# Performance work log

Hardware: AMD Instinct MI355X
Metric: run time of the kernel (lower is better)

The kernel has to match this reference:

```python
import jax, jax.numpy as jnp
import numpy as np

N = 50000
E = 400000
C_IN = 32
H = 64
RATIO = 0.5
SEQ_LEN = 5


def setup_inputs() -> dict:
    key = jax.random.key(0)
    ks = jax.random.split(key, 12)
    x = jax.random.normal(ks[0], (N, C_IN), jnp.float32)
    row = jax.random.randint(ks[1], (E,), 0, N, jnp.int32)
    off = jax.random.randint(ks[2], (E,), 1, N, jnp.int32)
    col = ((row + off) % N).astype(jnp.int32)  # no self-loops
    edge_index = jnp.stack([row, col])
    mask = jax.random.uniform(ks[3], (N,)) < 0.5

    def g(k, shape, fan):
        return jax.random.normal(k, shape, jnp.float32) / np.float32(np.sqrt(fan))

    return {
        "x": x, "edge_index": edge_index, "mask": mask,
        "conv0_w": g(ks[4], (C_IN, H), C_IN), "conv0_b": jnp.zeros((H,), jnp.float32),
        "conv1_w": g(ks[5], (H, H), H), "conv1_b": jnp.zeros((H,), jnp.float32),
        "pool_w": g(ks[6], (H,), H),
        "up_w": g(ks[7], (H, H), H), "up_b": jnp.zeros((H,), jnp.float32),
        "lstm0_w_ih": g(ks[8], (4 * H, H), H), "lstm0_w_hh": g(ks[9], (4 * H, H), H),
        "lstm0_b_ih": jnp.zeros((4 * H,), jnp.float32), "lstm0_b_hh": jnp.zeros((4 * H,), jnp.float32),
        "fin_w_ih": g(ks[10], (4 * H, H), H), "fin_w_hh": g(ks[11], (4 * H, H), H),
        "fin_b_ih": jnp.zeros((4 * H,), jnp.float32), "fin_b_hh": jnp.zeros((4 * H,), jnp.float32),
    }


def _coalesce(row, col, w, n):
    # sum duplicate (row, col) entries; output sorted by (row, col)
    key = row.astype(np.int64) * n + col.astype(np.int64)
    uk, inv = np.unique(key, return_inverse=True)
    w2 = np.bincount(inv, weights=w.astype(np.float64), minlength=uk.shape[0]).astype(np.float32)
    return uk // n, uk % n, w2


def _augment_adj(row, col, w, n):
    # remove self loops, add self loops (weight 1), compute A @ A (sparse), remove self loops
    m = row != col
    row = np.concatenate([row[m].astype(np.int64), np.arange(n, dtype=np.int64)])
    col = np.concatenate([col[m].astype(np.int64), np.arange(n, dtype=np.int64)])
    w = np.concatenate([w[m].astype(np.float32), np.ones(n, np.float32)])
    row, col, w = _coalesce(row, col, w, n)  # CSR-ordered
    cnt = np.bincount(row, minlength=n)
    indptr = np.concatenate([[0], np.cumsum(cnt)])
    dk = cnt[col]                      # out-degree of middle node k for each edge (i,k)
    starts = indptr[col]
    total = int(dk.sum())
    seg = np.repeat(np.cumsum(dk) - dk, dk)
    gi = np.repeat(starts, dk) + (np.arange(total) - seg)
    oi = np.repeat(row, dk)
    oj = col[gi]
    ow = np.repeat(w, dk) * w[gi]
    r2, c2, w2 = _coalesce(oi, oj, ow, n)
    m2 = r2 != c2
    return r2[m2], c2[m2], w2[m2]


def _gcn(x, row, col, ew, n, W, b):
    # GCNConv(improved=True): self-loop weight 2.0, symmetric deg^-1/2 normalization,
    # aggregate messages at target (col)
    h = x @ W
    loop = jnp.arange(n, dtype=row.dtype)
    r = jnp.concatenate([row, loop])
    c = jnp.concatenate([col, loop])
    w = jnp.concatenate([ew, jnp.full((n,), 2.0, ew.dtype)])
    deg = jax.ops.segment_sum(w, c, num_segments=n)
    dinv = jnp.where(deg > 0, jax.lax.rsqrt(deg), 0.0)
    norm = dinv[r] * w * dinv[c]
    out = jax.ops.segment_sum(norm[:, None] * h[r], c, num_segments=n)
    return out + b


def _sequences(x, mi):
    # sliding window [idx-L+1, idx] per masked node, zero left-padded
    t = mi[:, None] + jnp.arange(SEQ_LEN)[None, :] - (SEQ_LEN - 1)  # [M, L]
    return jnp.where((t >= 0)[:, :, None], x[jnp.clip(t, 0)], 0.0)


def _lstm_last(seq, w_ih, w_hh, b_ih, b_hh):
    # torch LSTM gate order: i, f, g, o; zero init state; return last hidden
    h = jnp.zeros((seq.shape[0], w_hh.shape[1]), seq.dtype)
    c = jnp.zeros_like(h)
    def step(carry, xt):
        h, c = carry
        g = xt @ w_ih.T + h @ w_hh.T + b_ih + b_hh
        i, f, gg, o = jnp.split(g, 4, axis=-1)
        c = jax.nn.sigmoid(f) * c + jax.nn.sigmoid(i) * jnp.tanh(gg)
        h = jax.nn.sigmoid(o) * jnp.tanh(c)
        return (h, c), None
    (h, _), _ = jax.lax.scan(step, (h, c), jnp.swapaxes(seq, 0, 1))
    return h


def reference(x, edge_index, mask, conv0_w, conv0_b, conv1_w, conv1_b, pool_w,
              up_w, up_b, lstm0_w_ih, lstm0_w_hh, lstm0_b_ih, lstm0_b_hh,
              fin_w_ih, fin_w_hh, fin_b_ih, fin_b_hh):
    n = x.shape[0]
    row0, col0 = edge_index[0], edge_index[1]
    ew0 = jnp.ones((row0.shape[0],), x.dtype)

    # down conv 0
    x1 = jax.nn.relu(_gcn(x, row0, col0, ew0, n, conv0_w, conv0_b))

    # augment_adj: sparse (A+I)^2 without diagonal (structural, constant)
    r2, c2, w2 = _augment_adj(np.asarray(row0), np.asarray(col0),
                              np.ones(row0.shape[0], np.float32), n)

    # TopKPooling: score = tanh((x.w)/||w||), keep top ceil(ratio*n)
    score = jnp.tanh((x1 @ pool_w) / jnp.linalg.norm(pool_w))
    k = int(np.ceil(RATIO * n))
    perm = np.argsort(-np.asarray(score), kind="stable")[:k]
    remap = np.full(n, -1, np.int64)
    remap[perm] = np.arange(k)
    keep = (remap[r2] >= 0) & (remap[c2] >= 0)
    pr = jnp.asarray(remap[r2[keep]].astype(np.int32))
    pc = jnp.asarray(remap[c2[keep]].astype(np.int32))
    pw = jnp.asarray(w2[keep])
    permj = jnp.asarray(perm.astype(np.int32))
    xp = x1[permj] * score[permj][:, None]

    # down conv 1 on pooled graph
    x2 = jax.nn.relu(_gcn(xp, pr, pc, pw, k, conv1_w, conv1_b))

    # up path (depth=1): LSTM over skip features at masked nodes
    mi = jnp.asarray(np.where(np.asarray(mask))[0].astype(np.int32))
    h0 = _lstm_last(_sequences(x1, mi), lstm0_w_ih, lstm0_w_hh, lstm0_b_ih, lstm0_b_hh)
    res = x1.at[mi].set(h0)
    up = jnp.zeros_like(x1).at[permj].set(x2)
    xo = _gcn(res + up, row0, col0, ew0, n, up_w, up_b)  # last level: no activation

    # final LSTM on masked nodes
    hf = _lstm_last(_sequences(xo, mi), fin_w_ih, fin_w_hh, fin_b_ih, fin_b_hh)
    return xo.at[mi].set(hf)
```

## Files before the change

kernel.cpp:

```cpp
#include <hip/hip_runtime.h>
#include <math.h>

#define NN 50000
#define EE 400000
#define CINV 32
#define KKEEP 25000
#define SEQL 5
#define HASH_BITS 20
#define HASH_SIZE (1u<<HASH_BITS)
#define HASH_MASK (HASH_SIZE-1u)
#define HEMPTY 0xFFFFFFFFu
#define PSB 196

typedef float vf4 __attribute__((ext_vector_type(4)));

__device__ __forceinline__ float sigm(float x){ return __builtin_amdgcn_rcpf(1.f+__expf(-x)); }
__device__ __forceinline__ float ftanh(float x){ return 1.f - 2.f*__builtin_amdgcn_rcpf(1.f+__expf(2.f*x)); }

__global__ void k_init(uint2* __restrict__ hash, unsigned* __restrict__ hist,
                       int* __restrict__ degcnt, int* __restrict__ diagint,
                       int* __restrict__ fillc, int* __restrict__ minv,
                       unsigned* scal, unsigned long long* selp,
                       const float* __restrict__ w0, const float* __restrict__ b0i,
                       const float* __restrict__ b0h, const float* __restrict__ wf,
                       const float* __restrict__ bfi, const float* __restrict__ bfh,
                       float* __restrict__ WT0, float* __restrict__ WTf,
                       float* __restrict__ bs0, float* __restrict__ bsf){
  int i = blockIdx.x*256 + threadIdx.x;
  if (i < (int)HASH_SIZE) hash[i] = make_uint2(HEMPTY, 0u);
  if (i < 4*65536) hist[i] = 0u;
  if (i < NN){ degcnt[i]=0; diagint[i]=0; fillc[i]=0; minv[i]=-1; }
  if (i < 256*64){
    int g = i>>6, k = i&63;
    WT0[k*256+g] = w0[i];
    WTf[k*256+g] = wf[i];
  }
  if (i < 256){ bs0[i]=b0i[i]+b0h[i]; bsf[i]=bfi[i]+bfh[i]; }
  if (i == 0){ scal[0]=0u; scal[1]=0u; scal[3]=KKEEP; selp[0]=0ull; }
}

__global__ void k_phase2(const int* __restrict__ row, const int* __restrict__ col,
                         const int* __restrict__ mp, int* __restrict__ degcnt,
                         uint2* __restrict__ tab, unsigned* scal){
  int e = blockIdx.x*256 + threadIdx.x;
  if (e < EE){
    int c = col[e];
    atomicAdd(&degcnt[c], 1);
    unsigned key = (unsigned)row[e]*50000u + (unsigned)c;
    unsigned h = (key*2654435761u) >> (32-HASH_BITS);
    for(;;){
      unsigned old = atomicCAS(&tab[h].x, HEMPTY, key);
      if (old==HEMPTY || old==key){ atomicAdd(&tab[h].y, 1u); break; }
      h = (h+1)&HASH_MASK;
    }
  }
  if (e < NN/4){ if ((unsigned)mp[e] > 1u) atomicOr(&scal[1], 1u); }
}

__global__ void k_psum1(const int* __restrict__ deg, int* __restrict__ part,
                        int* __restrict__ bsum, float* __restrict__ dinv){
  __shared__ int sc[256];
  int b = blockIdx.x, t = threadIdx.x, i = b*256+t;
  int v = (i<NN) ? deg[i] : 0;
  if (i < NN) dinv[i] = rsqrtf((float)v + 2.0f);
  sc[t] = v; __syncthreads();
  for (int o=1;o<256;o<<=1){
    int x = (t>=o) ? sc[t-o] : 0;
    __syncthreads();
    sc[t] += x;
    __syncthreads();
  }
  if (i < NN) part[i] = sc[t]-v;
  if (t == 255) bsum[b] = sc[255];
}
__global__ void k_psum2(const int* __restrict__ bsum, int* __restrict__ boff){
  __shared__ int sc[256];
  int t = threadIdx.x;
  int v = (t<PSB) ? bsum[t] : 0;
  sc[t] = v; __syncthreads();
  for (int o=1;o<256;o<<=1){
    int x = (t>=o) ? sc[t-o] : 0;
    __syncthreads();
    sc[t] += x;
    __syncthreads();
  }
  if (t < PSB) boff[t] = sc[t]-v;
}
__global__ void k_psum3(const int* __restrict__ part, const int* __restrict__ boff,
                        int* __restrict__ indptr){
  int i = blockIdx.x*256 + threadIdx.x;
  if (i < NN) indptr[i] = part[i] + boff[blockIdx.x];
  if (i == 0) indptr[NN] = EE;
}

__global__ void k_phase4(const int* __restrict__ row, const int* __restrict__ col,
                         const int* __restrict__ indptr, int* __restrict__ fillc,
                         int* __restrict__ csr_r, const uint2* __restrict__ tab,
                         int* __restrict__ diagint, const void* __restrict__ mp,
                         unsigned* scal, int* __restrict__ mlist, int* __restrict__ minv){
  int idx = blockIdx.x*256 + threadIdx.x;
  if (idx < EE){
    int r = row[idx], c = col[idx];
    int pos = indptr[c] + atomicAdd(&fillc[c], 1);
    csr_r[pos] = r;
    unsigned rkey = (unsigned)c*50000u + (unsigned)r;
    unsigned h = (rkey*2654435761u) >> (32-HASH_BITS);
    for(;;){
      unsigned kk = tab[h].x;
      if (kk==rkey){ atomicAdd(&diagint[r], (int)tab[h].y); break; }
      if (kk==HEMPTY) break;
      h = (h+1)&HASH_MASK;
    }
  } else {
    int i = idx - EE;
    if (i < NN){
      int mv = scal[1] ? (int)((const unsigned char*)mp)[i] : ((const int*)mp)[i];
      if (mv){ int p = (int)atomicAdd(&scal[0], 1u); mlist[p] = i; minv[i] = p; }
    }
  }
}

__global__ void k_mm_h0v(const float* __restrict__ X, const float* __restrict__ W, float* __restrict__ Y){
  int idx = blockIdx.x*256 + threadIdx.x;
  if (idx >= NN*16) return;
  int i = idx>>4, fq = idx&15;
  const vf4* X4 = (const vf4*)&X[i*CINV];
  const vf4* W4 = (const vf4*)W;
  vf4 acc = {0.f,0.f,0.f,0.f};
  #pragma unroll
  for (int kq=0;kq<CINV/4;kq++){
    vf4 xv = X4[kq];
    #pragma unroll
    for (int u=0;u<4;u++) acc += xv[u] * W4[(kq*4+u)*16+fq];
  }
  ((vf4*)Y)[i*16+fq] = acc;
}
__global__ void k_mm64v(const float* __restrict__ X, const float* __restrict__ W, float* __restrict__ Y){
  int idx = blockIdx.x*256 + threadIdx.x;
  if (idx >= NN*16) return;
  int i = idx>>4, fq = idx&15;
  const vf4* X4 = (const vf4*)&X[i*64];
  const vf4* W4 = (const vf4*)W;
  vf4 acc = {0.f,0.f,0.f,0.f};
  #pragma unroll
  for (int kq=0;kq<16;kq++){
    vf4 xv = X4[kq];
    #pragma unroll
    for (int u=0;u<4;u++) acc += xv[u] * W4[(kq*4+u)*16+fq];
  }
  ((vf4*)Y)[i*16+fq] = acc;
}
__global__ void k_mm64sv(const float* __restrict__ X, const float* __restrict__ W,
                         const float* __restrict__ sc, const int* __restrict__ kp,
                         float* __restrict__ Y){
  int idx = blockIdx.x*256 + threadIdx.x;
  if (idx >= NN*16) return;
  int i = idx>>4, fq = idx&15;
  if (!kp[i]) return;
  const vf4* X4 = (const vf4*)&X[i*64];
  const vf4* W4 = (const vf4*)W;
  vf4 acc = {0.f,0.f,0.f,0.f};
  #pragma unroll
  for (int kq=0;kq<16;kq++){
    vf4 xv = X4[kq];
    #pragma unroll
    for (int u=0;u<4;u++) acc += xv[u] * W4[(kq*4+u)*16+fq];
  }
  float s = sc[i];
  acc *= s;
  ((vf4*)Y)[i*16+fq] = acc;
}

__global__ void g_gcn0(const int* __restrict__ indptr, const int* __restrict__ csr_r,
                       const float* __restrict__ dinv, const float* __restrict__ H,
                       const float* __restrict__ b, const float* __restrict__ pw,
                       float* __restrict__ out, unsigned long long* __restrict__ keys,
                       float* __restrict__ score, unsigned* __restrict__ hist){
  int node = blockIdx.x*4 + (threadIdx.x>>6), lane = threadIdx.x&63;
  if (node >= NN) return;
  int s = __builtin_amdgcn_readfirstlane(indptr[node]);
  int e = __builtin_amdgcn_readfirstlane(indptr[node+1]);
  float acc = 0.f;
  for (int j=s;j<e;j++){
    int r = __builtin_amdgcn_readfirstlane(csr_r[j]);
    acc += dinv[r]*H[r*64+lane];
  }
  float di = dinv[node];
  float v = di*acc + 2.f*di*di*H[node*64+lane] + b[lane];
  float x1v = fmaxf(v, 0.f);
  out[node*64+lane] = x1v;
  float pv = pw[lane];
  float nq = pv*pv;
  float dq = x1v*pv;
  for (int o=32;o;o>>=1){ nq += __shfl_down(nq, o, 64); dq += __shfl_down(dq, o, 64); }
  if (lane==0){
    float sv = tanhf(dq / sqrtf(nq));
    sv = sv + 0.0f;
    score[node] = sv;
    unsigned u = __float_as_uint(sv);
    unsigned asc = (u>>31) ? ~u : (u | 0x80000000u);
    unsigned desc = ~asc;
    keys[node] = (((unsigned long long)desc)<<32) | (unsigned)node;
    atomicAdd(&hist[desc>>16], 1u);
  }
}
__global__ void g_t2(const int* __restrict__ indptr, const int* __restrict__ csr_r,
                     const float* __restrict__ dinv1, const float* __restrict__ hp,
                     float* __restrict__ t2){
  int node = blockIdx.x*4 + (threadIdx.x>>6), lane = threadIdx.x&63;
  if (node >= NN) return;
  int s = __builtin_amdgcn_readfirstlane(indptr[node]);
  int e = __builtin_amdgcn_readfirstlane(indptr[node+1]);
  float acc = dinv1[node]*hp[node*64+lane];
  for (int j=s;j<e;j++){
    int r = __builtin_amdgcn_readfirstlane(csr_r[j]);
    float dr = dinv1[r];
    if (dr != 0.f) acc += dr*hp[r*64+lane];
  }
  t2[node*64+lane] = acc;
}
__global__ void g_agg2y(const int* __restrict__ indptr, const int* __restrict__ csr_r,
                        const float* __restrict__ t2, const float* __restrict__ hp,
                        const float* __restrict__ dinv1, const int* __restrict__ diagint,
                        const int* __restrict__ kp, const float* __restrict__ b1,
                        const float* __restrict__ C, const float* __restrict__ Hbuf,
                        const int* __restrict__ minv, float* __restrict__ D){
  int node = blockIdx.x*4 + (threadIdx.x>>6), lane = threadIdx.x&63;
  if (node >= NN) return;
  int mv = minv[node];
  float base = (mv >= 0) ? Hbuf[(size_t)mv*64+lane] : C[node*64+lane];
  float add = 0.f;
  if (kp[node]){
    int s = __builtin_amdgcn_readfirstlane(indptr[node]);
    int e = __builtin_amdgcn_readfirstlane(indptr[node+1]);
    float acc = t2[node*64+lane];
    for (int j=s;j<e;j++){
      int r = __builtin_amdgcn_readfirstlane(csr_r[j]);
      acc += t2[r*64+lane];
    }
    float di = dinv1[node], hv = hp[node*64+lane];
    float diag = (float)(diagint[node] + 1);
    float v = di*(acc - diag*di*hv) + 2.f*di*di*hv + b1[lane];
    add = fmaxf(v, 0.f);
  }
  D[node*64+lane] = base + add;
}
__global__ void g_up(const int* __restrict__ indptr, const int* __restrict__ csr_r,
                     const float* __restrict__ dinv, const float* __restrict__ H,
                     const float* __restrict__ b, float* __restrict__ xo, float* __restrict__ out){
  int node = blockIdx.x*4 + (threadIdx.x>>6), lane = threadIdx.x&63;
  if (node >= NN) return;
  int s = __builtin_amdgcn_readfirstlane(indptr[node]);
  int e = __builtin_amdgcn_readfirstlane(indptr[node+1]);
  float acc = 0.f;
  for (int j=s;j<e;j++){
    int r = __builtin_amdgcn_readfirstlane(csr_r[j]);
    acc += dinv[r]*H[r*64+lane];
  }
  float di = dinv[node];
  float v = di*acc + 2.f*di*di*H[node*64+lane] + b[lane];
  xo[node*64+lane] = v; out[node*64+lane] = v;
}

__global__ void k_hist(const unsigned long long* __restrict__ keys, unsigned* __restrict__ hist,
                       const unsigned long long* __restrict__ selp, int round){
  int i = blockIdx.x*256 + threadIdx.x;
  if (i >= NN) return;
  unsigned long long key = keys[i];
  int shift = 48 - 16*round;
  if ((key>>(shift+16)) == selp[0])
    atomicAdd(&hist[(unsigned)((key>>shift)&0xFFFFull)], 1u);
}
__global__ void k_pick(const unsigned* __restrict__ hist, unsigned long long* selp, unsigned* scal){
  __shared__ unsigned csum[256];
  __shared__ unsigned bins[256];
  __shared__ int schunk;
  int t = threadIdx.x;
  const uint4* h4 = (const uint4*)(hist + t*256);
  unsigned s = 0;
  #pragma unroll 8
  for (int j=0;j<64;j++){ uint4 v = h4[j]; s += v.x+v.y+v.z+v.w; }
  csum[t] = s;
  __syncthreads();
  if (t==0){
    unsigned rem = scal[3];
    int chunk = 255;
    for (int c2=0;c2<256;c2++){ unsigned cc=csum[c2]; if (rem>cc) rem-=cc; else { chunk=c2; break; } }
    schunk = chunk; scal[3] = rem;
  }
  __syncthreads();
  bins[t] = hist[schunk*256 + t];
  __syncthreads();
  if (t==0){
    unsigned rem = scal[3];
    int bin = schunk*256 + 255;
    for (int b=0;b<256;b++){ unsigned hv=bins[b]; if (rem>hv) rem-=hv; else { bin = schunk*256 + b; break; } }
    selp[0] = (selp[0]<<16) | (unsigned long long)(unsigned)bin;
    scal[3] = rem;
  }
}
__global__ void k_tsg(const int* __restrict__ indptr, const int* __restrict__ csr_r,
                      const unsigned long long* __restrict__ keys,
                      const unsigned long long* __restrict__ selp,
                      int* __restrict__ kp, int* __restrict__ ts){
  int i = blockIdx.x*256 + threadIdx.x;
  if (i >= NN) return;
  unsigned long long sp = selp[0];
  int s = indptr[i], e = indptr[i+1];
  int self = (keys[i] <= sp) ? 1 : 0;
  kp[i] = self;
  int acc = self;
  for (int j=s;j<e;j++) acc += (keys[csr_r[j]] <= sp) ? 1 : 0;
  ts[i] = acc;
}
__global__ void k_csg(const int* __restrict__ indptr, const int* __restrict__ csr_r,
                      const int* __restrict__ ts, const int* __restrict__ diagint,
                      const int* __restrict__ kp, float* __restrict__ dinv1){
  int i = blockIdx.x*256 + threadIdx.x;
  if (i >= NN) return;
  int s = indptr[i], e = indptr[i+1];
  int acc = ts[i];
  for (int j=s;j<e;j++) acc += ts[csr_r[j]];
  dinv1[i] = kp[i] ? rsqrtf((float)(acc - diagint[i] - 1) + 2.0f) : 0.f;
}

__global__ __launch_bounds__(256) void k_xw(const float* __restrict__ src,
        const float* __restrict__ WT, const float* __restrict__ bsum,
        float* __restrict__ XW){
  __shared__ vf4 Wl[4096];
  int t = threadIdx.x;
  const vf4* Wg = (const vf4*)WT;
  for (int u=t; u<4096; u+=256) Wl[u] = Wg[u];
  int fq = t & 63, wv = t >> 6;
  vf4 bias = ((const vf4*)bsum)[fq];
  __syncthreads();
  for (int g = blockIdx.x*4 + wv; g < NN/4; g += gridDim.x*4){
    int n0 = g*4;
    const vf4* X4 = (const vf4*)&src[(size_t)n0*64];
    vf4 a0=bias, a1=bias, a2=bias, a3=bias;
    #pragma unroll 4
    for (int kq=0;kq<16;kq++){
      vf4 x0 = X4[kq], x1 = X4[16+kq], x2 = X4[32+kq], x3 = X4[48+kq];
      vf4 w0 = Wl[(kq*4+0)*64+fq];
      vf4 w1 = Wl[(kq*4+1)*64+fq];
      vf4 w2 = Wl[(kq*4+2)*64+fq];
      vf4 w3 = Wl[(kq*4+3)*64+fq];
      a0 += x0.x*w0 + x0.y*w1 + x0.z*w2 + x0.w*w3;
      a1 += x1.x*w0 + x1.y*w1 + x1.z*w2 + x1.w*w3;
      a2 += x2.x*w0 + x2.y*w1 + x2.z*w2 + x2.w*w3;
      a3 += x3.x*w0 + x3.y*w1 + x3.z*w2 + x3.w*w3;
    }
    vf4* Y = (vf4*)XW;
    Y[(size_t)n0*64 + fq]       = a0;
    Y[(size_t)n0*64 + 64 + fq]  = a1;
    Y[(size_t)n0*64 + 128 + fq] = a2;
    Y[(size_t)n0*64 + 192 + fq] = a3;
  }
}

__global__ __launch_bounds__(256) void k_rec(const float* __restrict__ XW,
        const float* __restrict__ whh, const float* __restrict__ bsum,
        const int* __restrict__ mlist, const unsigned* __restrict__ scal,
        float* __restrict__ dst, int scatter){
  int M = (int)scal[0];
  if (M < 0 || M > NN) M = 0;
  int w = threadIdx.x>>6, lane = threadIdx.x&63;
  int r = w*64 + lane;
  const vf4* g4 = (const vf4*)&whh[(size_t)r*64];
  vf4 wh[16];
  #pragma unroll
  for (int j=0;j<16;j++) wh[j] = g4[j];
  __shared__ float sh[4][64];
  __shared__ float gates[4][4][64];
  int ntask = (M+3)>>2;
  for (int task = blockIdx.x; task < ntask; task += gridDim.x){
    int m = task*4 + w;
    bool valid = (m < M);
    int node = mlist[valid ? m : (M-1)];
    node = min(max(node, 0), NN-1);
    float c, h;
    float x0,x1,x2,x3;
    {
      int rowi = node - (SEQL-1);
      if (rowi >= 0){
        const float* p = &XW[(size_t)rowi*256];
        x0=p[lane]; x1=p[64+lane]; x2=p[128+lane]; x3=p[192+lane];
      } else {
        x0=bsum[lane]; x1=bsum[64+lane]; x2=bsum[128+lane]; x3=bsum[192+lane];
      }
      c = sigm(x0)*ftanh(x2);
      h = sigm(x3)*ftanh(c);
      sh[w][lane] = h;
    }
    __syncthreads();
    for (int t=1;t<SEQL;t++){
      int rowi = node - (SEQL-1) + t;
      if (rowi >= 0){
        const float* p = &XW[(size_t)rowi*256];
        x0=p[lane]; x1=p[64+lane]; x2=p[128+lane]; x3=p[192+lane];
      } else {
        x0=bsum[lane]; x1=bsum[64+lane]; x2=bsum[128+lane]; x3=bsum[192+lane];
      }
      vf4 a0={0,0,0,0}, a1={0,0,0,0}, a2={0,0,0,0}, a3={0,0,0,0};
      #pragma unroll
      for (int j=0;j<16;j++){
        vf4 wj = wh[j];
        a0 += (*(const vf4*)&sh[0][j*4]) * wj;
        a1 += (*(const vf4*)&sh[1][j*4]) * wj;
        a2 += (*(const vf4*)&sh[2][j*4]) * wj;
        a3 += (*(const vf4*)&sh[3][j*4]) * wj;
      }
      gates[0][w][lane] = a0.x+a0.y+a0.z+a0.w;
      gates[1][w][lane] = a1.x+a1.y+a1.z+a1.w;
      gates[2][w][lane] = a2.x+a2.y+a2.z+a2.w;
      gates[3][w][lane] = a3.x+a3.y+a3.z+a3.w;
      __syncthreads();
      float gi = gates[w][0][lane] + x0;
      float gf = gates[w][1][lane] + x1;
      float gg = gates[w][2][lane] + x2;
      float go = gates[w][3][lane] + x3;
      c = sigm(gf)*c + sigm(gi)*ftanh(gg);
      h = sigm(go)*ftanh(c);
      sh[w][lane] = h;
      __syncthreads();
    }
    if (valid){
      size_t o = scatter ? ((size_t)node*64 + lane) : ((size_t)m*64 + lane);
      dst[o] = h;
    }
  }
}

extern "C" void kernel_launch(void* const* d_in, const int* in_sizes, int n_in,
                              void* d_out, int out_size, void* d_ws, size_t ws_size,
                              hipStream_t stream) {
  const float* x   = (const float*)d_in[0];
  const int*   ei  = (const int*)d_in[1];
  const int*   row = ei;
  const int*   col = ei + EE;
  const void*  mp  = d_in[2];
  const float* W0  = (const float*)d_in[3];
  const float* b0  = (const float*)d_in[4];
  const float* W1  = (const float*)d_in[5];
  const float* b1  = (const float*)d_in[6];
  const float* pw  = (const float*)d_in[7];
  const float* Wu  = (const float*)d_in[8];
  const float* bu  = (const float*)d_in[9];
  const float* l0wih=(const float*)d_in[10];
  const float* l0whh=(const float*)d_in[11];
  const float* l0bih=(const float*)d_in[12];
  const float* l0bhh=(const float*)d_in[13];
  const float* lfwih=(const float*)d_in[14];
  const float* lfwhh=(const float*)d_in[15];
  const float* lfbih=(const float*)d_in[16];
  const float* lfbhh=(const float*)d_in[17];

  char* wp = (char*)d_ws;
  auto alloc = [&](size_t bytes)->char*{ char* p = wp; wp += ((bytes+255)/256)*256; return p; };
  float* A     = (float*)alloc((size_t)NN*64*4);
  float* B     = (float*)alloc((size_t)NN*64*4);
  float* C     = (float*)alloc((size_t)NN*64*4);
  float* D     = (float*)alloc((size_t)NN*64*4);
  float* Ebuf  = (float*)alloc((size_t)NN*64*4);
  float* Hbuf  = (float*)alloc((size_t)NN*64*4);
  float* XW    = (float*)alloc((size_t)NN*256*4);
  float* WT0   = (float*)alloc((size_t)256*64*4);
  float* WTf   = (float*)alloc((size_t)256*64*4);
  float* bs0   = (float*)alloc((size_t)256*4);
  float* bsf   = (float*)alloc((size_t)256*4);
  float* score = (float*)alloc((size_t)NN*4);
  float* dinv0 = (float*)alloc((size_t)NN*4);
  float* dinv1 = (float*)alloc((size_t)NN*4);
  unsigned long long* keys = (unsigned long long*)alloc((size_t)NN*8);
  int* degcnt  = (int*)alloc((size_t)NN*4);
  int* diagint = (int*)alloc((size_t)NN*4);
  int* ts      = (int*)alloc((size_t)NN*4);
  int* kp      = (int*)alloc((size_t)NN*4);
  int* mlist   = (int*)alloc((size_t)NN*4);
  int* minv    = (int*)alloc((size_t)NN*4);
  int* indptr  = (int*)alloc((size_t)(NN+1)*4);
  int* part    = (int*)alloc((size_t)NN*4);
  int* fillc   = (int*)alloc((size_t)NN*4);
  int* bsum    = (int*)alloc((size_t)256*4);
  int* boff    = (int*)alloc((size_t)256*4);
  int* csr_r   = (int*)alloc((size_t)EE*4);
  uint2* hash  = (uint2*)alloc((size_t)HASH_SIZE*8);
  unsigned* hist=(unsigned*)alloc((size_t)4*65536*4);
  unsigned* scal=(unsigned*)alloc(256);
  unsigned long long* selp = (unsigned long long*)(scal + 4);

  #define GRID1(n) dim3(((n)+255)/256), dim3(256), 0, stream
  #define GRIDW dim3((NN+3)/4), dim3(256), 0, stream

  k_init<<<GRID1(HASH_SIZE)>>>(hash, hist, degcnt, diagint, fillc, minv,
                               scal, selp, l0wih, l0bih, l0bhh, lfwih, lfbih, lfbhh,
                               WT0, WTf, bs0, bsf);
  k_phase2<<<GRID1(EE)>>>(row, col, (const int*)mp, degcnt, hash, scal);
  k_psum1<<<dim3(PSB),dim3(256),0,stream>>>(degcnt, part, bsum, dinv0);
  k_psum2<<<dim3(1),dim3(256),0,stream>>>(bsum, boff);
  k_psum3<<<dim3(PSB),dim3(256),0,stream>>>(part, boff, indptr);
  k_phase4<<<GRID1(EE+NN)>>>(row, col, indptr, fillc, csr_r, hash, diagint, mp, scal, mlist, minv);

  k_mm_h0v<<<GRID1(NN*16)>>>(x, W0, A);
  g_gcn0<<<GRIDW>>>(indptr, csr_r, dinv0, A, b0, pw, C, keys, score, hist);

  k_pick<<<dim3(1),dim3(256),0,stream>>>(hist, selp, scal);
  for (int r2=1;r2<4;r2++){
    k_hist<<<GRID1(NN)>>>(keys, hist + r2*65536, selp, r2);
    k_pick<<<dim3(1),dim3(256),0,stream>>>(hist + r2*65536, selp, scal);
  }
  k_tsg<<<GRID1(NN)>>>(indptr, csr_r, keys, selp, kp, ts);
  k_csg<<<GRID1(NN)>>>(indptr, csr_r, ts, diagint, kp, dinv1);

  k_mm64sv<<<GRID1(NN*16)>>>(C, W1, score, kp, Ebuf);
  g_t2<<<GRIDW>>>(indptr, csr_r, dinv1, Ebuf, A);

  k_xw<<<dim3(512),dim3(256),0,stream>>>(C, WT0, bs0, XW);
  k_rec<<<dim3(2048),dim3(256),0,stream>>>(XW, l0whh, bs0, mlist, scal, Hbuf, 0);

  g_agg2y<<<GRIDW>>>(indptr, csr_r, A, Ebuf, dinv1, diagint, kp, b1, C, Hbuf, minv, D);

  k_mm64v<<<GRID1(NN*16)>>>(D, Wu, Ebuf);
  g_up<<<GRIDW>>>(indptr, csr_r, dinv0, Ebuf, bu, B, (float*)d_out);

  k_xw<<<dim3(512),dim3(256),0,stream>>>(B, WTf, bsf, XW);
  k_rec<<<dim3(2048),dim3(256),0,stream>>>(XW, lfwhh, bsf, mlist, scal, (float*)d_out, 1);
  #undef GRIDW
  #undef GRID1
}
```

Baseline: 702.4 us.

## Batch neighbor index loads with shuffles and double LSTM sequences per wave

In the four CSR gather kernels, each wave now loads up to 64 neighbor indices (and their degree scales) at once and broadcasts them with shuffles. Several independent accumulators let multiple row gathers be in flight together, replacing the serial scalar index load per edge. Separately, the LSTM recurrence kernel now gives each wave two sequences, so every block handles eight and the register-held recurrent weights are reused across twice as many hidden states per sync. The costs are more registers and shared memory, plus a changed floating-point summation order.

After: 688.7 us. Within noise of the previous version (-1.9%).

```diff
diff --git a/kernel.cpp b/kernel.cpp
--- a/kernel.cpp
+++ b/kernel.cpp
@@ -180,15 +180,32 @@
   if (node >= NN) return;
   int s = __builtin_amdgcn_readfirstlane(indptr[node]);
   int e = __builtin_amdgcn_readfirstlane(indptr[node+1]);
-  float acc = 0.f;
-  for (int j=s;j<e;j++){
-    int r = __builtin_amdgcn_readfirstlane(csr_r[j]);
-    acc += dinv[r]*H[r*64+lane];
-  }
+  int deg = e - s;
+  float a0=0.f,a1=0.f,a2=0.f,a3=0.f;
+  for (int base=0; base<deg; base+=64){
+    int take = min(64, deg-base);
+    bool act = lane < take;
+    int ii = act ? csr_r[s+base+lane] : 0;
+    float dv = act ? dinv[ii] : 0.f;
+    int j=0;
+    for (; j+4<=take; j+=4){
+      int r0=__shfl(ii,j,64), r1=__shfl(ii,j+1,64), r2=__shfl(ii,j+2,64), r3=__shfl(ii,j+3,64);
+      float d0=__shfl(dv,j,64), d1=__shfl(dv,j+1,64), d2=__shfl(dv,j+2,64), d3=__shfl(dv,j+3,64);
+      a0 += d0*H[(size_t)r0*64+lane];
+      a1 += d1*H[(size_t)r1*64+lane];
+      a2 += d2*H[(size_t)r2*64+lane];
+      a3 += d3*H[(size_t)r3*64+lane];
+    }
+    for (; j<take; j++){
+      int r0=__shfl(ii,j,64); float d0=__shfl(dv,j,64);
+      a0 += d0*H[(size_t)r0*64+lane];
+    }
+  }
+  float acc = (a0+a1)+(a2+a3);
   float di = dinv[node];
-  float v = di*acc + 2.f*di*di*H[node*64+lane] + b[lane];
+  float v = di*acc + 2.f*di*di*H[(size_t)node*64+lane] + b[lane];
   float x1v = fmaxf(v, 0.f);
-  out[node*64+lane] = x1v;
+  out[(size_t)node*64+lane] = x1v;
   float pv = pw[lane];
   float nq = pv*pv;
   float dq = x1v*pv;
@@ -211,13 +228,27 @@
   if (node >= NN) return;
   int s = __builtin_amdgcn_readfirstlane(indptr[node]);
   int e = __builtin_amdgcn_readfirstlane(indptr[node+1]);
-  float acc = dinv1[node]*hp[node*64+lane];
-  for (int j=s;j<e;j++){
-    int r = __builtin_amdgcn_readfirstlane(csr_r[j]);
-    float dr = dinv1[r];
-    if (dr != 0.f) acc += dr*hp[r*64+lane];
-  }
-  t2[node*64+lane] = acc;
+  int deg = e - s;
+  float a0 = dinv1[node]*hp[(size_t)node*64+lane];
+  float a1 = 0.f;
+  for (int base=0; base<deg; base+=64){
+    int take = min(64, deg-base);
+    bool act = lane < take;
+    int ii = act ? csr_r[s+base+lane] : 0;
+    float dv = act ? dinv1[ii] : 0.f;
+    int j=0;
+    for (; j+2<=take; j+=2){
+      float d0=__shfl(dv,j,64), d1=__shfl(dv,j+1,64);
+      int r0=__shfl(ii,j,64), r1=__shfl(ii,j+1,64);
+      if (d0!=0.f) a0 += d0*hp[(size_t)r0*64+lane];
+      if (d1!=0.f) a1 += d1*hp[(size_t)r1*64+lane];
+    }
+    for (; j<take; j++){
+      float d0=__shfl(dv,j,64); int r0=__shfl(ii,j,64);
+      if (d0!=0.f) a0 += d0*hp[(size_t)r0*64+lane];
+    }
+  }
+  t2[(size_t)node*64+lane] = a0+a1;
 }
 __global__ void g_agg2y(const int* __restrict__ indptr, const int* __restrict__ csr_r,
                         const float* __restrict__ t2, const float* __restrict__ hp,
@@ -228,22 +259,38 @@
   int node = blockIdx.x*4 + (threadIdx.x>>6), lane = threadIdx.x&63;
   if (node >= NN) return;
   int mv = minv[node];
-  float base = (mv >= 0) ? Hbuf[(size_t)mv*64+lane] : C[node*64+lane];
+  float base = (mv >= 0) ? Hbuf[(size_t)mv*64+lane] : C[(size_t)node*64+lane];
   float add = 0.f;
   if (kp[node]){
     int s = __builtin_amdgcn_readfirstlane(indptr[node]);
     int e = __builtin_amdgcn_readfirstlane(indptr[node+1]);
-    float acc = t2[node*64+lane];
-    for (int j=s;j<e;j++){
-      int r = __builtin_amdgcn_readfirstlane(csr_r[j]);
-      acc += t2[r*64+lane];
-    }
-    float di = dinv1[node], hv = hp[node*64+lane];
+    int deg = e - s;
+    float a0 = t2[(size_t)node*64+lane];
+    float a1=0.f,a2=0.f,a3=0.f;
+    for (int bs2=0; bs2<deg; bs2+=64){
+      int take = min(64, deg-bs2);
+      bool act = lane < take;
+      int ii = act ? csr_r[s+bs2+lane] : 0;
+      int j=0;
+      for (; j+4<=take; j+=4){
+        int r0=__shfl(ii,j,64), r1=__shfl(ii,j+1,64), r2=__shfl(ii,j+2,64), r3=__shfl(ii,j+3,64);
+        a0 += t2[(size_t)r0*64+lane];
+        a1 += t2[(size_t)r1*64+lane];
+        a2 += t2[(size_t)r2*64+lane];
+        a3 += t2[(size_t)r3*64+lane];
+      }
+      for (; j<take; j++){
+        int r0=__shfl(ii,j,64);
+        a0 += t2[(size_t)r0*64+lane];
+      }
+    }
+    float acc = (a0+a1)+(a2+a3);
+    float di = dinv1[node], hv = hp[(size_t)node*64+lane];
     float diag = (float)(diagint[node] + 1);
     float v = di*(acc - diag*di*hv) + 2.f*di*di*hv + b1[lane];
     add = fmaxf(v, 0.f);
   }
-  D[node*64+lane] = base + add;
+  D[(size_t)node*64+lane] = base + add;
 }
 __global__ void g_up(const int* __restrict__ indptr, const int* __restrict__ csr_r,
                      const float* __restrict__ dinv, const float* __restrict__ H,
@@ -252,14 +299,31 @@
   if (node >= NN) return;
   int s = __builtin_amdgcn_readfirstlane(indptr[node]);
   int e = __builtin_amdgcn_readfirstlane(indptr[node+1]);
-  float acc = 0.f;
-  for (int j=s;j<e;j++){
-    int r = __builtin_amdgcn_readfirstlane(csr_r[j]);
-    acc += dinv[r]*H[r*64+lane];
-  }
+  int deg = e - s;
+  float a0=0.f,a1=0.f,a2=0.f,a3=0.f;
+  for (int base=0; base<deg; base+=64){
+    int take = min(64, deg-base);
+    bool act = lane < take;
+    int ii = act ? csr_r[s+base+lane] : 0;
+    float dv = act ? dinv[ii] : 0.f;
+    int j=0;
+    for (; j+4<=take; j+=4){
+      int r0=__shfl(ii,j,64), r1=__shfl(ii,j+1,64), r2=__shfl(ii,j+2,64), r3=__shfl(ii,j+3,64);
+      float d0=__shfl(dv,j,64), d1=__shfl(dv,j+1,64), d2=__shfl(dv,j+2,64), d3=__shfl(dv,j+3,64);
+      a0 += d0*H[(size_t)r0*64+lane];
+      a1 += d1*H[(size_t)r1*64+lane];
+      a2 += d2*H[(size_t)r2*64+lane];
+      a3 += d3*H[(size_t)r3*64+lane];
+    }
+    for (; j<take; j++){
+      int r0=__shfl(ii,j,64); float d0=__shfl(dv,j,64);
+      a0 += d0*H[(size_t)r0*64+lane];
+    }
+  }
+  float acc = (a0+a1)+(a2+a3);
   float di = dinv[node];
-  float v = di*acc + 2.f*di*di*H[node*64+lane] + b[lane];
-  xo[node*64+lane] = v; out[node*64+lane] = v;
+  float v = di*acc + 2.f*di*di*H[(size_t)node*64+lane] + b[lane];
+  xo[(size_t)node*64+lane] = v; out[(size_t)node*64+lane] = v;
 }
 
 __global__ void k_hist(const unsigned long long* __restrict__ keys, unsigned* __restrict__ hist,
@@ -370,38 +434,46 @@
   vf4 wh[16];
   #pragma unroll
   for (int j=0;j<16;j++) wh[j] = g4[j];
-  __shared__ float sh[4][64];
-  __shared__ float gates[4][4][64];
-  int ntask = (M+3)>>2;
+  __shared__ float sh[8][64];
+  __shared__ float gates[8][4][64];
+  int ntask = (M+7)>>3;
   for (int task = blockIdx.x; task < ntask; task += gridDim.x){
-    int m = task*4 + w;
-    bool valid = (m < M);
-    int node = mlist[valid ? m : (M-1)];
-    node = min(max(node, 0), NN-1);
-    float c, h;
-    float x0,x1,x2,x3;
+    int m0 = task*8 + 2*w, m1 = m0+1;
+    bool v0 = (m0 < M), v1 = (m1 < M);
+    int n0 = mlist[v0 ? m0 : (M-1)];
+    int n1 = mlist[v1 ? m1 : (M-1)];
+    n0 = min(max(n0, 0), NN-1);
+    n1 = min(max(n1, 0), NN-1);
+    float c0, h0, c1, h1;
+    float x0,x1,x2,x3, y0,y1,y2,y3;
     {
-      int rowi = node - (SEQL-1);
-      if (rowi >= 0){
-        const float* p = &XW[(size_t)rowi*256];
+      int ra = n0 - (SEQL-1), rb = n1 - (SEQL-1);
+      if (ra >= 0){
+        const float* p = &XW[(size_t)ra*256];
         x0=p[lane]; x1=p[64+lane]; x2=p[128+lane]; x3=p[192+lane];
-      } else {
-        x0=bsum[lane]; x1=bsum[64+lane]; x2=bsum[128+lane]; x3=bsum[192+lane];
-      }
-      c = sigm(x0)*ftanh(x2);
-      h = sigm(x3)*ftanh(c);
-      sh[w][lane] = h;
+      } else { x0=bsum[lane]; x1=bsum[64+lane]; x2=bsum[128+lane]; x3=bsum[192+lane]; }
+      if (rb >= 0){
+        const float* p = &XW[(size_t)rb*256];
+        y0=p[lane]; y1=p[64+lane]; y2=p[128+lane]; y3=p[192+lane];
+      } else { y0=bsum[lane]; y1=bsum[64+lane]; y2=bsum[128+lane]; y3=bsum[192+lane]; }
+      c0 = sigm(x0)*ftanh(x2); h0 = sigm(x3)*ftanh(c0);
+      c1 = sigm(y0)*ftanh(y2); h1 = sigm(y3)*ftanh(c1);
+      sh[2*w][lane] = h0;
+      sh[2*w+1][lane] = h1;
     }
     __syncthreads();
     for (int t=1;t<SEQL;t++){
-      int rowi = node - (SEQL-1) + t;
-      if (rowi >= 0){
-        const float* p = &XW[(size_t)rowi*256];
+      int ra = n0 - (SEQL-1) + t, rb = n1 - (SEQL-1) + t;
+      if (ra >= 0){
+        const float* p = &XW[(size_t)ra*256];
         x0=p[lane]; x1=p[64+lane]; x2=p[128+lane]; x3=p[192+lane];
-      } else {
-        x0=bsum[lane]; x1=bsum[64+lane]; x2=bsum[128+lane]; x3=bsum[192+lane];
-      }
-      vf4 a0={0,0,0,0}, a1={0,0,0,0}, a2={0,0,0,0}, a3={0,0,0,0};
+      } else { x0=bsum[lane]; x1=bsum[64+lane]; x2=bsum[128+lane]; x3=bsum[192+lane]; }
+      if (rb >= 0){
+        const float* p = &XW[(size_t)rb*256];
+        y0=p[lane]; y1=p[64+lane]; y2=p[128+lane]; y3=p[192+lane];
+      } else { y0=bsum[lane]; y1=bsum[64+lane]; y2=bsum[128+lane]; y3=bsum[192+lane]; }
+      vf4 a0={0,0,0,0},a1={0,0,0,0},a2={0,0,0,0},a3={0,0,0,0};
+      vf4 a4={0,0,0,0},a5={0,0,0,0},a6={0,0,0,0},a7={0,0,0,0};
       #pragma unroll
       for (int j=0;j<16;j++){
         vf4 wj = wh[j];
@@ -409,24 +481,44 @@
         a1 += (*(const vf4*)&sh[1][j*4]) * wj;
         a2 += (*(const vf4*)&sh[2][j*4]) * wj;
         a3 += (*(const vf4*)&sh[3][j*4]) * wj;
+        a4 += (*(const vf4*)&sh[4][j*4]) * wj;
+        a5 += (*(const vf4*)&sh[5][j*4]) * wj;
+        a6 += (*(const vf4*)&sh[6][j*4]) * wj;
+        a7 += (*(const vf4*)&sh[7][j*4]) * wj;
       }
       gates[0][w][lane] = a0.x+a0.y+a0.z+a0.w;
       gates[1][w][lane] = a1.x+a1.y+a1.z+a1.w;
       gates[2][w][lane] = a2.x+a2.y+a2.z+a2.w;
       gates[3][w][lane] = a3.x+a3.y+a3.z+a3.w;
+      gates[4][w][lane] = a4.x+a4.y+a4.z+a4.w;
+      gates[5][w][lane] = a5.x+a5.y+a5.z+a5.w;
+      gates[6][w][lane] = a6.x+a6.y+a6.z+a6.w;
+      gates[7][w][lane] = a7.x+a7.y+a7.z+a7.w;
       __syncthreads();
-      float gi = gates[w][0][lane] + x0;
-      float gf = gates[w][1][lane] + x1;
-      float gg = gates[w][2][lane] + x2;
-      float go = gates[w][3][lane] + x3;
-      c = sigm(gf)*c + sigm(gi)*ftanh(gg);
-      h = sigm(go)*ftanh(c);
-      sh[w][lane] = h;
+      int p0 = 2*w, p1 = 2*w+1;
+      float gi = gates[p0][0][lane] + x0;
+      float gf = gates[p0][1][lane] + x1;
+      float gg = gates[p0][2][lane] + x2;
+      float go = gates[p0][3][lane] + x3;
+      c0 = sigm(gf)*c0 + sigm(gi)*ftanh(gg);
+      h0 = sigm(go)*ftanh(c0);
+      sh[p0][lane] = h0;
+      gi = gates[p1][0][lane] + y0;
+      gf = gates[p1][1][lane] + y1;
+      gg = gates[p1][2][lane] + y2;
+      go = gates[p1][3][lane] + y3;
+      c1 = sigm(gf)*c1 + sigm(gi)*ftanh(gg);
+      h1 = sigm(go)*ftanh(c1);
+      sh[p1][lane] = h1;
       __syncthreads();
     }
-    if (valid){
-      size_t o = scatter ? ((size_t)node*64 + lane) : ((size_t)m*64 + lane);
-      dst[o] = h;
+    if (v0){
+      size_t o = scatter ? ((size_t)n0*64 + lane) : ((size_t)m0*64 + lane);
+      dst[o] = h0;
+    }
+    if (v1){
+      size_t o = scatter ? ((size_t)n1*64 + lane) : ((size_t)m1*64 + lane);
+      dst[o] = h1;
     }
   }
 }
```
